# Performance work log

Measured on AMD Instinct MI355X. Metric: run time of the kernel, lower is better.

Reference implementation:

```python
import jax, jax.numpy as jnp
import numpy as np

N_PTS = 131072      # query points
N_DIMS = 3          # spatial dims
N_FEATS = 1000      # total_n_features = prod(feature_grid_shape '10,10,10')
FDIM = 64           # n_features per grid point
PE_TERMS = 6        # num_positional_encoding_terms
HID = 128           # nodes_per_layer
OUT = 1             # n_outputs
D_IN = PE_TERMS * N_DIMS * 2 + FDIM  # 100


def _linear_init(k, d_in, d_out):
    # xavier-ish init for a [out, in] torch-style weight
    return jax.random.normal(k, (d_out, d_in), dtype=jnp.float32) * np.float32(1.0 / np.sqrt(d_in))


def setup_inputs() -> dict:
    key = jax.random.key(0)
    ks = jax.random.split(key, 10)
    x = jax.random.uniform(ks[0], (N_PTS, N_DIMS), minval=-1.0, maxval=1.0, dtype=jnp.float32)
    feature_locations = jax.random.uniform(ks[1], (N_FEATS, N_DIMS), minval=-1.0, maxval=1.0, dtype=jnp.float32)
    feature_vectors = jax.random.normal(ks[2], (N_FEATS, FDIM), dtype=jnp.float32)
    W0 = _linear_init(ks[3], D_IN, HID); b0 = jnp.zeros((HID,), jnp.float32)
    W1 = _linear_init(ks[4], HID, HID);  b1 = jnp.zeros((HID,), jnp.float32)
    W2 = _linear_init(ks[5], HID, HID);  b2 = jnp.zeros((HID,), jnp.float32)
    W3 = _linear_init(ks[6], HID, HID);  b3 = jnp.zeros((HID,), jnp.float32)
    W4 = _linear_init(ks[7], HID, OUT);  b4 = jnp.zeros((OUT,), jnp.float32)
    return dict(x=x, feature_locations=feature_locations, feature_vectors=feature_vectors,
                W0=W0, b0=b0, W1=W1, b1=b1, W2=W2, b2=b2, W3=W3, b3=b3, W4=W4, b4=b4)


def _snake_alt(h):
    # SnakeAlt activation: 0.5*x + sin(x)^2
    return 0.5 * h + jnp.sin(h) ** 2


def _positional_encoding(x):
    # NeRF-style PE: sin/cos of (2^l * pi * x), l = 0..PE_TERMS-1 -> [N, PE_TERMS*N_DIMS*2]
    freqs = (2.0 ** jnp.arange(PE_TERMS, dtype=jnp.float32)) * jnp.pi
    ang = x[:, :, None] * freqs  # [N, n_dims, L]
    return jnp.concatenate([jnp.sin(ang), jnp.cos(ang)], axis=-1).reshape(x.shape[0], -1)


def reference(x, feature_locations, feature_vectors, W0, b0, W1, b1, W2, b2, W3, b3, W4, b4):
    # L2 distance from each point to each feature location, via expanded quadratic form
    # (same math as sqrt(sum((x-loc)^2)) without materializing [N, F, n_dims])
    d2 = (jnp.sum(x * x, axis=-1, keepdims=True)
          - 2.0 * (x @ feature_locations.T)
          + jnp.sum(feature_locations * feature_locations, axis=-1))
    d2 = jnp.maximum(d2, 0.0)
    inv_d = 1.0 / (jnp.sqrt(d2) + 1e-6)
    w = jax.nn.softmax(inv_d, axis=1)            # [N, F]
    feats = w @ feature_vectors                  # [N, FDIM]
    pe = _positional_encoding(x)                 # [N, 36]
    y = jnp.concatenate([pe, feats], axis=1)     # [N, 100]
    y = _snake_alt(y @ W0.T + b0)
    y = _snake_alt(y @ W1.T + b1)
    y = _snake_alt(y @ W2.T + b2)
    y = _snake_alt(y @ W3.T + b3)
    return y @ W4.T + b4                         # [N, 1]
```

## Files before the change

### kernel.cpp

```cpp
#include <hip/hip_runtime.h>
#include <hip/hip_bf16.h>

#define N_PTS   131072
#define N_FEATS 1000
#define FDIM    64
#define HID     128
#define NCHUNK  32
#define PI_F    3.14159265358979f
#define L2E     1.44269504f
#define EPS_D2  4e-7f

typedef short  short8  __attribute__((ext_vector_type(8)));
typedef float  floatx4 __attribute__((ext_vector_type(4)));

__device__ __forceinline__ unsigned int packbf2(float a, float b) {
    float2 t; t.x = a; t.y = b;
    __hip_bfloat162 h = __float22bfloat162_rn(t);
    union { __hip_bfloat162 hh; unsigned int u; } cv; cv.hh = h;
    return cv.u;
}
__device__ __forceinline__ unsigned short f2bf(float f) {
    return (unsigned short)packbf2(f, f);
}
__device__ __forceinline__ float bf2f(unsigned short h) {
    return __uint_as_float(((unsigned int)h) << 16);
}
__device__ __forceinline__ floatx4 min3_4(floatx4 a, floatx4 b, floatx4 c) {
    floatx4 r;
    r[0] = fminf(fminf(a[0], b[0]), c[0]);
    r[1] = fminf(fminf(a[1], b[1]), c[1]);
    r[2] = fminf(fminf(a[2], b[2]), c[2]);
    r[3] = fminf(fminf(a[3], b[3]), c[3]);
    return r;
}
__device__ __forceinline__ unsigned int pack_p2(float d0, float d1, float nm) {
    float p0 = __builtin_amdgcn_exp2f(fmaf(__builtin_amdgcn_rsqf(d0), L2E, nm));
    float p1 = __builtin_amdgcn_exp2f(fmaf(__builtin_amdgcn_rsqf(d1), L2E, nm));
    return packbf2(p0, p1);
}


__device__ __forceinline__ short8 xfrag_build(int quad, float x0, float x1, float x2) {
    unsigned short h0, m0, l0, h1, m1, l1, h2, m2, l2, Ah, Am, Al;
    { h0 = f2bf(x0); float r = x0 - bf2f(h0); m0 = f2bf(r); l0 = f2bf(r - bf2f(m0)); }
    { h1 = f2bf(x1); float r = x1 - bf2f(h1); m1 = f2bf(r); l1 = f2bf(r - bf2f(m1)); }
    { h2 = f2bf(x2); float r = x2 - bf2f(h2); m2 = f2bf(r); l2 = f2bf(r - bf2f(m2)); }
    float A = x0*x0 + x1*x1 + x2*x2;
    { Ah = f2bf(A); float r = A - bf2f(Ah); Am = f2bf(r); Al = f2bf(r - bf2f(Am)); }
    union { short8 v; unsigned short u[8]; } f;
    if (quad == 0) {
        f.u[0]=h0; f.u[1]=m0; f.u[2]=h0; f.u[3]=l0; f.u[4]=m0; f.u[5]=h0; f.u[6]=h1; f.u[7]=m1;
    } else if (quad == 1) {
        f.u[0]=h1; f.u[1]=l1; f.u[2]=m1; f.u[3]=h1; f.u[4]=h2; f.u[5]=m2; f.u[6]=h2; f.u[7]=l2;
    } else if (quad == 2) {
        f.u[0]=m2; f.u[1]=h2; f.u[2]=0x3F80; f.u[3]=0x3F80; f.u[4]=0x3F80; f.u[5]=Ah; f.u[6]=Am; f.u[7]=Al;
    } else {
        f.v = (short8)0;
        f.u[0] = 0x3F80;
    }
    return f.v;
}

__global__ void prep_all(const float* __restrict__ locs, const float* __restrict__ fv,
                         const float* __restrict__ W0, const float* __restrict__ W1,
                         const float* __restrict__ W2, const float* __restrict__ W3,
                         unsigned short* __restrict__ DB,
                         unsigned short* __restrict__ fvB, unsigned short* __restrict__ WB)
{
    int i = blockIdx.x * 256 + threadIdx.x;
    if (i < 65536) {
        int j = i & 7, n = (i >> 3) & 63, cq = i >> 9;
        int c = cq >> 2, quad = cq & 3;
        int fl = (j < 4) ? quad*4 + j : 16 + quad*4 + (j - 4);
        int f = c*32 + fl;
        float v = (f < N_FEATS) ? fv[f*FDIM + n] : 0.f;
        fvB[i] = f2bf(v);
    } else if (i < 131072) {
        int r = i - 65536;
        int j = r & 7, lane = (r >> 3) & 63, c = (r >> 9) & 3;
        int nt = (r >> 11) & 1, q = (r >> 12) & 3, L = r >> 14;
        int n = (q*2 + nt)*16 + (lane & 15);
        int k = c*32 + (lane >> 4)*8 + j;
        const float* W = (L == 0) ? W0 : (L == 1) ? W1 : (L == 2) ? W2 : W3;
        int Kin = (L == 0) ? 100 : 128;
        float v = (k < Kin) ? W[n*Kin + k] : 0.f;
        WB[r] = f2bf(v);
    } else if (i < 163840) {
        int r = i - 131072;
        int j = r & 7, ft = (r >> 3) & 15, quad = (r >> 7) & 3, fg = r >> 9;
        int f = fg*16 + ft, s = quad*8 + j;
        float lx, ly, lz;
        if (f < N_FEATS) { lx = locs[f*3+0]; ly = locs[f*3+1]; lz = locs[f*3+2]; }
        else             { lx = 1e9f; ly = 1e9f; lz = 1e9f; }
        unsigned short val = 0;
        if (s < 18) {
            int d = s / 6, t = s - d*6;
            float l2 = -2.f * ((d == 0) ? lx : (d == 1) ? ly : lz);
            unsigned short h = f2bf(l2);
            float r1 = l2 - bf2f(h);
            unsigned short m = f2bf(r1);
            unsigned short l = f2bf(r1 - bf2f(m));
            val = (t == 2 || t == 4) ? m : (t == 5) ? l : h;
        } else if (s < 21) {
            float SL = lx*lx + ly*ly + lz*lz;
            unsigned short h = f2bf(SL);
            float r1 = SL - bf2f(h);
            unsigned short m = f2bf(r1);
            unsigned short l = f2bf(r1 - bf2f(m));
            val = (s == 18) ? h : (s == 19) ? m : l;
        } else if (s < 24) {
            val = 0x3F80;
        } else if (s == 24) {
            val = f2bf(EPS_D2);
        }
        DB[r] = val;
    }
}

__global__ __launch_bounds__(256, 4)
void afvsrn_mfma(const float* __restrict__ x,
                 const unsigned short* __restrict__ DB,
                 const unsigned short* __restrict__ fvB,
                 const unsigned short* __restrict__ WB,
                 const float* __restrict__ b0, const float* __restrict__ b1,
                 const float* __restrict__ b2, const float* __restrict__ b3,
                 const float* __restrict__ W4, const float* __restrict__ b4,
                 float* __restrict__ out)
{
    __shared__ unsigned short act[128 * 136];

    const int lane = threadIdx.x & 63;
    const int wv   = threadIdx.x >> 6;
    const int ptl  = lane & 15;
    const int quad = lane >> 4;
    const int ptbase = blockIdx.x * 128 + wv * 32;

    float x0[2], x1[2], x2[2];
    #pragma unroll
    for (int t = 0; t < 2; ++t) {
        x0[t] = x[(ptbase + t*16 + ptl)*3 + 0];
        x1[t] = x[(ptbase + t*16 + ptl)*3 + 1];
        x2[t] = x[(ptbase + t*16 + ptl)*3 + 2];
    }
    short8 xf[2];
    #pragma unroll
    for (int t = 0; t < 2; ++t) xf[t] = xfrag_build(quad, x0[t], x1[t], x2[t]);

    const short8* DBp = (const short8*)DB;
    const int dbidx = quad*16 + ptl;
    const floatx4 Z = {0.f, 0.f, 0.f, 0.f};

    floatx4 mn[2];
    #pragma unroll
    for (int t = 0; t < 2; ++t) { mn[t][0]=1e30f; mn[t][1]=1e30f; mn[t][2]=1e30f; mn[t][3]=1e30f; }
    #pragma unroll 2
    for (int c = 0; c < NCHUNK; ++c) {
        short8 a0 = DBp[(2*c    )*64 + dbidx];
        short8 a1 = DBp[(2*c + 1)*64 + dbidx];
        #pragma unroll
        for (int t = 0; t < 2; ++t) {
            floatx4 d0 = __builtin_amdgcn_mfma_f32_16x16x32_bf16(a0, xf[t], Z, 0, 0, 0);
            floatx4 d1 = __builtin_amdgcn_mfma_f32_16x16x32_bf16(a1, xf[t], Z, 0, 0, 0);
            mn[t] = min3_4(mn[t], d0, d1);
        }
    }
    float nm[2];
    #pragma unroll
    for (int t = 0; t < 2; ++t) {
        float md = fminf(fminf(mn[t][0], mn[t][1]), fminf(mn[t][2], mn[t][3]));
        md = fminf(md, __shfl_xor(md, 16));
        md = fminf(md, __shfl_xor(md, 32));
        nm[t] = -__builtin_amdgcn_rsqf(md) * L2E;
    }

    const short8 ONES = {0x3F80,0x3F80,0x3F80,0x3F80,0x3F80,0x3F80,0x3F80,0x3F80};
    floatx4 acc2[2][4] = {};
    floatx4 accL[2] = {};
    #pragma unroll 1
    for (int c = 0; c < NCHUNK-1; ++c) {
        const short8* bp = (const short8*)fvB + (c*4 + quad)*64;
        short8 bfv0 = bp[ptl];
        short8 bfv1 = bp[16 + ptl];
        short8 bfv2 = bp[32 + ptl];
        short8 bfv3 = bp[48 + ptl];
        short8 a0 = DBp[(2*c    )*64 + dbidx];
        short8 a1 = DBp[(2*c + 1)*64 + dbidx];
        #pragma unroll
        for (int t = 0; t < 2; ++t) {
            floatx4 d0 = __builtin_amdgcn_mfma_f32_16x16x32_bf16(a0, xf[t], Z, 0, 0, 0);
            floatx4 d1 = __builtin_amdgcn_mfma_f32_16x16x32_bf16(a1, xf[t], Z, 0, 0, 0);
            union { short8 v; unsigned int u[4]; } af;
            af.u[0] = pack_p2(d0[0], d0[1], nm[t]);
            af.u[1] = pack_p2(d0[2], d0[3], nm[t]);
            af.u[2] = pack_p2(d1[0], d1[1], nm[t]);
            af.u[3] = pack_p2(d1[2], d1[3], nm[t]);
            acc2[t][0] = __builtin_amdgcn_mfma_f32_16x16x32_bf16(af.v, bfv0, acc2[t][0], 0, 0, 0);
            acc2[t][1] = __builtin_amdgcn_mfma_f32_16x16x32_bf16(af.v, bfv1, acc2[t][1], 0, 0, 0);
            acc2[t][2] = __builtin_amdgcn_mfma_f32_16x16x32_bf16(af.v, bfv2, acc2[t][2], 0, 0, 0);
            acc2[t][3] = __builtin_amdgcn_mfma_f32_16x16x32_bf16(af.v, bfv3, acc2[t][3], 0, 0, 0);
            accL[t]    = __builtin_amdgcn_mfma_f32_16x16x32_bf16(af.v, ONES, accL[t], 0, 0, 0);
        }
    }
    {
        const int c = NCHUNK-1;
        const short8* bp = (const short8*)fvB + (c*4 + quad)*64;
        short8 bfv0 = bp[ptl];
        short8 bfv1 = bp[16 + ptl];
        short8 bfv2 = bp[32 + ptl];
        short8 bfv3 = bp[48 + ptl];
        short8 a0 = DBp[(2*c)*64 + dbidx];
        #pragma unroll
        for (int t = 0; t < 2; ++t) {
            floatx4 d0 = __builtin_amdgcn_mfma_f32_16x16x32_bf16(a0, xf[t], Z, 0, 0, 0);
            const float nme = (quad < 2) ? nm[t] : -__builtin_inff();
            union { short8 v; unsigned int u[4]; } af;
            af.u[0] = pack_p2(d0[0], d0[1], nme);
            af.u[1] = pack_p2(d0[2], d0[3], nme);
            af.u[2] = 0; af.u[3] = 0;
            acc2[t][0] = __builtin_amdgcn_mfma_f32_16x16x32_bf16(af.v, bfv0, acc2[t][0], 0, 0, 0);
            acc2[t][1] = __builtin_amdgcn_mfma_f32_16x16x32_bf16(af.v, bfv1, acc2[t][1], 0, 0, 0);
            acc2[t][2] = __builtin_amdgcn_mfma_f32_16x16x32_bf16(af.v, bfv2, acc2[t][2], 0, 0, 0);
            acc2[t][3] = __builtin_amdgcn_mfma_f32_16x16x32_bf16(af.v, bfv3, acc2[t][3], 0, 0, 0);
            accL[t]    = __builtin_amdgcn_mfma_f32_16x16x32_bf16(af.v, ONES, accL[t], 0, 0, 0);
        }
    }

    float linv[2][4];
    #pragma unroll
    for (int t = 0; t < 2; ++t)
        #pragma unroll
        for (int r = 0; r < 4; ++r)
            linv[t][r] = __builtin_amdgcn_rcpf(accL[t][r]);

    int myrow[2];
    #pragma unroll
    for (int t = 0; t < 2; ++t) {
        myrow[t] = (wv*32 + t*16 + ptl) * 136;
        *(short8*)&act[myrow[t] + 96 + quad*8] = (short8)0;
    }

    #pragma unroll
    for (int i = 0; i < 9; ++i) {
        int k = quad*9 + i;
        int d = k / 12, r12 = k % 12, l = r12 % 6;
        float fr = PI_F * (float)(1 << l);
        #pragma unroll
        for (int t = 0; t < 2; ++t) {
            float xv = (d == 0) ? x0[t] : (d == 1) ? x1[t] : x2[t];
            float v = (r12 < 6) ? __sinf(xv * fr) : __cosf(xv * fr);
            act[myrow[t] + k] = f2bf(v);
        }
    }

    #pragma unroll
    for (int nt = 0; nt < 4; ++nt)
        #pragma unroll
        for (int r = 0; r < 4; ++r)
            #pragma unroll
            for (int t = 0; t < 2; ++t)
                act[(wv*32 + t*16 + quad*4 + r)*136 + 36 + nt*16 + ptl] =
                    f2bf(acc2[t][nt][r] * linv[t][r]);

    short8 a[2][4];
    #pragma unroll 1
    for (int st = 0; st < 16; ++st) {
        const int L = st >> 2, q = st & 3;
        if (q == 0) {
            #pragma unroll
            for (int t = 0; t < 2; ++t)
                #pragma unroll
                for (int c = 0; c < 4; ++c)
                    a[t][c] = *(const short8*)&act[myrow[t] + c*32 + quad*8];
        }
        const float* bL = (L == 0) ? b0 : (L == 1) ? b1 : (L == 2) ? b2 : b3;
        const short8* bp = (const short8*)WB + st*512;
        #pragma unroll
        for (int nt = 0; nt < 2; ++nt) {
            floatx4 ac[2] = {};
            #pragma unroll
            for (int c = 0; c < 4; ++c) {
                short8 bw = bp[(nt*4 + c)*64 + lane];
                #pragma unroll
                for (int t = 0; t < 2; ++t)
                    ac[t] = __builtin_amdgcn_mfma_f32_16x16x32_bf16(a[t][c], bw, ac[t], 0, 0, 0);
            }
            const int col = (q*2 + nt)*16 + ptl;
            const float bias = bL[col];
            #pragma unroll
            for (int t = 0; t < 2; ++t)
                #pragma unroll
                for (int r = 0; r < 4; ++r) {
                    float h = ac[t][r] + bias;
                    float s = __sinf(h);
                    h = 0.5f*h + s*s;
                    act[(wv*32 + t*16 + quad*4 + r)*136 + col] = f2bf(h);
                }
        }
    }

    float o[2] = {0.f, 0.f};
    #pragma unroll
    for (int sg = 0; sg < 4; ++sg) {
        const floatx4* wp = (const floatx4*)W4 + (quad*32 + sg*8)/4;
        floatx4 w0 = wp[0], w1 = wp[1];
        #pragma unroll
        for (int t = 0; t < 2; ++t) {
            short8 av = *(const short8*)&act[myrow[t] + quad*32 + sg*8];
            o[t] = fmaf(bf2f((unsigned short)av[0]), w0[0], o[t]);
            o[t] = fmaf(bf2f((unsigned short)av[1]), w0[1], o[t]);
            o[t] = fmaf(bf2f((unsigned short)av[2]), w0[2], o[t]);
            o[t] = fmaf(bf2f((unsigned short)av[3]), w0[3], o[t]);
            o[t] = fmaf(bf2f((unsigned short)av[4]), w1[0], o[t]);
            o[t] = fmaf(bf2f((unsigned short)av[5]), w1[1], o[t]);
            o[t] = fmaf(bf2f((unsigned short)av[6]), w1[2], o[t]);
            o[t] = fmaf(bf2f((unsigned short)av[7]), w1[3], o[t]);
        }
    }
    #pragma unroll
    for (int t = 0; t < 2; ++t) {
        o[t] += __shfl_xor(o[t], 16);
        o[t] += __shfl_xor(o[t], 32);
    }
    if (quad == 0) {
        float bb = b4[0];
        #pragma unroll
        for (int t = 0; t < 2; ++t)
            out[ptbase + t*16 + ptl] = o[t] + bb;
    }
}

extern "C" void kernel_launch(void* const* d_in, const int* in_sizes, int n_in,
                              void* d_out, int out_size, void* d_ws, size_t ws_size,
                              hipStream_t stream)
{
    const float* x  = (const float*)d_in[0];
    const float* lc = (const float*)d_in[1];
    const float* fv = (const float*)d_in[2];
    const float* W0 = (const float*)d_in[3];
    const float* b0 = (const float*)d_in[4];
    const float* W1 = (const float*)d_in[5];
    const float* b1 = (const float*)d_in[6];
    const float* W2 = (const float*)d_in[7];
    const float* b2 = (const float*)d_in[8];
    const float* W3 = (const float*)d_in[9];
    const float* b3 = (const float*)d_in[10];
    const float* W4 = (const float*)d_in[11];
    const float* b4 = (const float*)d_in[12];

    char* ws = (char*)d_ws;
    unsigned short* DBp = (unsigned short*)(ws + 0);
    unsigned short* fvB = (unsigned short*)(ws + 65536);
    unsigned short* WB  = (unsigned short*)(ws + 65536 + 131072);

    prep_all<<<dim3(640), dim3(256), 0, stream>>>(lc, fv, W0, W1, W2, W3,
                                                  DBp, fvB, WB);

    afvsrn_mfma<<<dim3(N_PTS/128), dim3(256), 0, stream>>>(
        x, DBp, fvB, WB, b0, b1, b2, b3, W4, b4, (float*)d_out);
}
```

Before: 151.2 us.

## Replace separate min-distance pass with online softmax using deferred rescaling

Result: no change. 153.7 us (+1.7%).

```diff
diff --git a/kernel.cpp b/kernel.cpp
--- a/kernel.cpp
+++ b/kernel.cpp
@@ -9,6 +9,7 @@
 #define PI_F    3.14159265358979f
 #define L2E     1.44269504f
 #define EPS_D2  4e-7f
+#define DEFER_IV 11.0f
 
 typedef short  short8  __attribute__((ext_vector_type(8)));
 typedef float  floatx4 __attribute__((ext_vector_type(4)));
@@ -24,14 +25,6 @@
 }
 __device__ __forceinline__ float bf2f(unsigned short h) {
     return __uint_as_float(((unsigned int)h) << 16);
-}
-__device__ __forceinline__ floatx4 min3_4(floatx4 a, floatx4 b, floatx4 c) {
-    floatx4 r;
-    r[0] = fminf(fminf(a[0], b[0]), c[0]);
-    r[1] = fminf(fminf(a[1], b[1]), c[1]);
-    r[2] = fminf(fminf(a[2], b[2]), c[2]);
-    r[3] = fminf(fminf(a[3], b[3]), c[3]);
-    return r;
 }
 __device__ __forceinline__ unsigned int pack_p2(float d0, float d1, float nm) {
     float p0 = __builtin_amdgcn_exp2f(fmaf(__builtin_amdgcn_rsqf(d0), L2E, nm));
@@ -150,32 +143,13 @@
     const int dbidx = quad*16 + ptl;
     const floatx4 Z = {0.f, 0.f, 0.f, 0.f};
 
-    floatx4 mn[2];
-    #pragma unroll
-    for (int t = 0; t < 2; ++t) { mn[t][0]=1e30f; mn[t][1]=1e30f; mn[t][2]=1e30f; mn[t][3]=1e30f; }
-    #pragma unroll 2
-    for (int c = 0; c < NCHUNK; ++c) {
-        short8 a0 = DBp[(2*c    )*64 + dbidx];
-        short8 a1 = DBp[(2*c + 1)*64 + dbidx];
-        #pragma unroll
-        for (int t = 0; t < 2; ++t) {
-            floatx4 d0 = __builtin_amdgcn_mfma_f32_16x16x32_bf16(a0, xf[t], Z, 0, 0, 0);
-            floatx4 d1 = __builtin_amdgcn_mfma_f32_16x16x32_bf16(a1, xf[t], Z, 0, 0, 0);
-            mn[t] = min3_4(mn[t], d0, d1);
-        }
-    }
-    float nm[2];
-    #pragma unroll
-    for (int t = 0; t < 2; ++t) {
-        float md = fminf(fminf(mn[t][0], mn[t][1]), fminf(mn[t][2], mn[t][3]));
-        md = fminf(md, __shfl_xor(md, 16));
-        md = fminf(md, __shfl_xor(md, 32));
-        nm[t] = -__builtin_amdgcn_rsqf(md) * L2E;
-    }
-
     const short8 ONES = {0x3F80,0x3F80,0x3F80,0x3F80,0x3F80,0x3F80,0x3F80,0x3F80};
     floatx4 acc2[2][4] = {};
     floatx4 accL[2] = {};
+    float md_l[2] = {1e30f, 1e30f};
+    float nm[2]   = {0.f, 0.f};
+    float thr[2]  = {1e30f, 1e30f};
+
     #pragma unroll 1
     for (int c = 0; c < NCHUNK-1; ++c) {
         const short8* bp = (const short8*)fvB + (c*4 + quad)*64;
@@ -189,6 +163,27 @@
         for (int t = 0; t < 2; ++t) {
             floatx4 d0 = __builtin_amdgcn_mfma_f32_16x16x32_bf16(a0, xf[t], Z, 0, 0, 0);
             floatx4 d1 = __builtin_amdgcn_mfma_f32_16x16x32_bf16(a1, xf[t], Z, 0, 0, 0);
+            float mc = fminf(fminf(fminf(d0[0], d0[1]), fminf(d0[2], d0[3])),
+                             fminf(fminf(d1[0], d1[1]), fminf(d1[2], d1[3])));
+            md_l[t] = fminf(md_l[t], mc);
+            if (__any(md_l[t] < thr[t])) {
+                float mp = md_l[t];
+                mp = fminf(mp, __shfl_xor(mp, 16));
+                mp = fminf(mp, __shfl_xor(mp, 32));
+                float m_new  = __builtin_amdgcn_rsqf(mp);
+                float nm_new = -m_new * L2E;
+                float dl     = nm_new - nm[t];
+                #pragma unroll
+                for (int r = 0; r < 4; ++r) {
+                    float f = __builtin_amdgcn_exp2f(__shfl(dl, quad*4 + r));
+                    acc2[t][0][r] *= f; acc2[t][1][r] *= f;
+                    acc2[t][2][r] *= f; acc2[t][3][r] *= f;
+                    accL[t][r]    *= f;
+                }
+                nm[t] = nm_new;
+                float mt = m_new + DEFER_IV;
+                thr[t] = __builtin_amdgcn_rcpf(mt * mt);
+            }
             union { short8 v; unsigned int u[4]; } af;
             af.u[0] = pack_p2(d0[0], d0[1], nm[t]);
             af.u[1] = pack_p2(d0[2], d0[3], nm[t]);
@@ -212,6 +207,24 @@
         #pragma unroll
         for (int t = 0; t < 2; ++t) {
             floatx4 d0 = __builtin_amdgcn_mfma_f32_16x16x32_bf16(a0, xf[t], Z, 0, 0, 0);
+            float mc = fminf(fminf(d0[0], d0[1]), fminf(d0[2], d0[3]));
+            md_l[t] = fminf(md_l[t], mc);
+            if (__any(md_l[t] < thr[t])) {
+                float mp = md_l[t];
+                mp = fminf(mp, __shfl_xor(mp, 16));
+                mp = fminf(mp, __shfl_xor(mp, 32));
+                float m_new  = __builtin_amdgcn_rsqf(mp);
+                float nm_new = -m_new * L2E;
+                float dl     = nm_new - nm[t];
+                #pragma unroll
+                for (int r = 0; r < 4; ++r) {
+                    float f = __builtin_amdgcn_exp2f(__shfl(dl, quad*4 + r));
+                    acc2[t][0][r] *= f; acc2[t][1][r] *= f;
+                    acc2[t][2][r] *= f; acc2[t][3][r] *= f;
+                    accL[t][r]    *= f;
+                }
+                nm[t] = nm_new;
+            }
             const float nme = (quad < 2) ? nm[t] : -__builtin_inff();
             union { short8 v; unsigned int u[4]; } af;
             af.u[0] = pack_p2(d0[0], d0[1], nme);
```
